# Optimization experiments

Hardware: AMD Instinct MI355X
Metric: run time of the kernel (lower is better)

Reference implementation:

```python
import jax, jax.numpy as jnp
import numpy as np

# Config (mirrors MarketBDHConfig / BDHConfig defaults used here)
B, T = 2, 512
NUM_ASSETS, IN_FEAT = 93, 4
D = 256          # n_embd
NH = 4           # n_head
MULT = 64        # mlp_internal_dim_multiplier
NL = 6           # n_layer
NI = D * MULT // NH  # per-head internal dim N = 4096
IN_DIM = NUM_ASSETS * IN_FEAT  # 372
ROPE_THETA = 2.0 ** 16
EPS = 1e-5


def _ln(x):
    # LayerNorm over last dim, elementwise_affine=False
    m = jnp.mean(x, axis=-1, keepdims=True)
    v = jnp.mean(jnp.square(x - m), axis=-1, keepdims=True)
    return (x - m) * jax.lax.rsqrt(v + EPS)


def _rope(x, cos, sin):
    # x: [B,NH,T,NI]; cos/sin: [T, NI//2] (broadcast over B,NH)
    x1, x2 = x[..., 0::2], x[..., 1::2]
    out = jnp.stack([x1 * cos - x2 * sin, x1 * sin + x2 * cos], axis=-1)
    return out.reshape(x.shape)


def setup_inputs() -> dict:
    key = jax.random.key(0)
    ks = jax.random.split(key, 9)
    s = 0.02
    return {
        "x": jax.random.normal(ks[0], (B, T, NUM_ASSETS, IN_FEAT), jnp.float32),
        "in_W": jax.random.normal(ks[1], (IN_DIM, D), jnp.float32) * s,
        "in_b": jnp.zeros((D,), jnp.float32),
        "encoder": jax.random.normal(ks[2], (NH, D, NI), jnp.float32) * s,
        "encoder_v": jax.random.normal(ks[3], (NH, D, NI), jnp.float32) * s,
        "decoder": jax.random.normal(ks[4], (NH * NI, D), jnp.float32) * s,
        "head_W": jax.random.normal(ks[5], (D, IN_DIM), jnp.float32) * s,
        "head_b": jnp.zeros((IN_DIM,), jnp.float32),
    }


def reference(x, in_W, in_b, encoder, encoder_v, decoder, head_W, head_b):
    # input projection: [B,T,N,F] -> [B,T,IN_DIM] -> [B,T,D]
    x_flat = x.reshape(B, T, IN_DIM)
    h = _ln(x_flat @ in_W + in_b)  # [B,T,D]

    # RoPE phase tables over the internal (latent) dimension
    freqs = 1.0 / (ROPE_THETA ** (jnp.arange(0, NI, 2, dtype=jnp.float32) / NI))
    phases = jnp.arange(T, dtype=jnp.float32)[:, None] * freqs[None, :]  # [T, NI/2]
    cos, sin = jnp.cos(phases), jnp.sin(phases)

    dec = decoder.reshape(NH, NI, D)  # head-major flatten matches transpose(1,2).reshape

    for _ in range(NL):
        h_res = h
        # encode + relu-sparsify: [B,NH,T,NI]
        h_sparse = jax.nn.relu(jnp.einsum('btd,hdn->bhtn', h, encoder))
        # BDH attention: linear (no softmax), K is Q, is_causal=False -> dense scores
        qr = _rope(h_sparse, cos, sin)
        scores = jnp.einsum('bhtn,bhsn->bhts', qr, qr)  # [B,NH,T,T]
        yKV = jnp.einsum('bhts,bsd->bhtd', scores, h)    # V = h broadcast over heads
        yKV = _ln(yKV)
        y_sparse = jax.nn.relu(jnp.einsum('bhtd,hdn->bhtn', yKV, encoder_v))
        xy_sparse = h_sparse * y_sparse  # multiplicative gating (dropout p=0)
        yMLP = jnp.einsum('bhtn,hnd->btd', xy_sparse, dec)
        h = _ln(h_res + _ln(yMLP))

    pred = (h @ head_W + head_b).reshape(B, T, NUM_ASSETS, IN_FEAT)
    return pred
```

## Files before the change

### kernel.cpp

```cpp
#include <hip/hip_runtime.h>
#include <math.h>

#define B_ 2
#define T_ 512
#define D_ 256
#define NH_ 4
#define NI_ 4096
#define IN_DIM_ 372
#define NL_ 6
#define EPS_ 1e-5f

typedef unsigned short u16;
typedef __attribute__((ext_vector_type(4))) float f32x4;
typedef __attribute__((ext_vector_type(8))) short bf16x8;

__device__ __forceinline__ u16 f2b(float f) {
  union { float f; unsigned u; } v; v.f = f;
  unsigned r = v.u + 0x7fffu + ((v.u >> 16) & 1u);
  return (u16)(r >> 16);
}
__device__ __forceinline__ float b2f(u16 s) {
  union { unsigned u; float f; } v; v.u = ((unsigned)s) << 16;
  return v.f;
}

__device__ __forceinline__ void gload16(const u16* g, u16* l) {
  __builtin_amdgcn_global_load_lds(
      (const __attribute__((address_space(1))) unsigned int*)g,
      (__attribute__((address_space(3))) unsigned int*)l, 16, 0, 0);
}

__device__ __forceinline__ float blkSum256(float v, float* sb4) {
  #pragma unroll
  for (int o = 32; o > 0; o >>= 1) v += __shfl_down(v, o, 64);
  int w = threadIdx.x >> 6;
  __syncthreads();
  if ((threadIdx.x & 63) == 0) sb4[w] = v;
  __syncthreads();
  return sb4[0] + sb4[1] + sb4[2] + sb4[3];
}

__device__ __forceinline__ void gemm128(const u16* __restrict__ A,
                                        const u16* __restrict__ Bt,
                                        int lda, int k0, int k1,
                                        int row0, int col0,
                                        u16* Als, u16* Bls,
                                        f32x4 acc[4][4]) {
  const int tid = threadIdx.x;
  const int lane = tid & 63;
  const int wv = tid >> 6;
  const int wr = (wv >> 1) << 6;
  const int wc = (wv & 1) << 6;
  const int frow = lane & 15;
  const int kch = (lane >> 4) << 3;
  #pragma unroll
  for (int m = 0; m < 4; m++)
    #pragma unroll
    for (int n = 0; n < 4; n++) {
      f32x4 z = {0.f, 0.f, 0.f, 0.f};
      acc[m][n] = z;
    }
  for (int k = k0; k < k1; k += 32) {
    #pragma unroll
    for (int i = 0; i < 2; i++) {
      int s = tid + (i << 8);
      int r = s >> 2, c = (s & 3) << 3;
      gload16(A + (long)(row0 + r) * lda + k + c, Als + s * 8);
      gload16(Bt + (long)(col0 + r) * lda + k + c, Bls + s * 8);
    }
    __syncthreads();
    bf16x8 af[4], bfv[4];
    #pragma unroll
    for (int m = 0; m < 4; m++)
      af[m] = *(const bf16x8*)(Als + (wr + m * 16 + frow) * 32 + kch);
    #pragma unroll
    for (int n = 0; n < 4; n++)
      bfv[n] = *(const bf16x8*)(Bls + (wc + n * 16 + frow) * 32 + kch);
    #pragma unroll
    for (int m = 0; m < 4; m++)
      #pragma unroll
      for (int n = 0; n < 4; n++)
        acc[m][n] = __builtin_amdgcn_mfma_f32_16x16x32_bf16(af[m], bfv[n], acc[m][n], 0, 0, 0);
    __syncthreads();
  }
}

#define EPILOG_SETUP \
  const int lane = threadIdx.x & 63; \
  const int wv = threadIdx.x >> 6; \
  const int wr = (wv >> 1) << 6, wc = (wv & 1) << 6;

#define STAGE_HALF(EXPR) \
  if (wr == h * 64) { \
    _Pragma("unroll") \
    for (int m = 0; m < 4; m++) \
      _Pragma("unroll") \
      for (int n = 0; n < 4; n++) \
        _Pragma("unroll") \
        for (int r = 0; r < 4; r++) { \
          int lr = m * 16 + ((lane >> 4) << 2) + r; \
          int lc = wc + n * 16 + (lane & 15); \
          float _a = acc[m][n][r]; \
          smem[lr * 128 + (lc ^ (((lr >> 2) & 7) << 3))] = f2b(EXPR); \
        } \
  } \
  __syncthreads();

__device__ __forceinline__ void storeC_lds(const f32x4 acc[4][4], u16* smem,
                                           u16* Cb, int ldc, int row0, int col0,
                                           int wr, int wc, int lane) {
  const int tid = threadIdx.x;
  #pragma unroll
  for (int h = 0; h < 2; h++) {
    STAGE_HALF(_a)
    #pragma unroll
    for (int i = 0; i < 4; i++) {
      int idx = i * 256 + tid;
      int lr = idx >> 4, ch = idx & 15;
      uint4 v = *(const uint4*)(smem + lr * 128 + ((ch ^ ((lr >> 2) & 7)) << 3));
      *(uint4*)(Cb + (long)(row0 + h * 64 + lr) * ldc + col0 + ch * 8) = v;
    }
    __syncthreads();
  }
}

__global__ __launch_bounds__(256)
void k_cs(unsigned* __restrict__ cs) {
  int idx = blockIdx.x * 256 + threadIdx.x;
  if (idx >= T_ * (NI_ / 2)) return;
  int t = idx >> 11;
  int k = idx & 2047;
  float freq = exp2f(-(float)k * (1.0f / 128.0f));
  float ph = (float)t * freq;
  cs[idx] = (unsigned)f2b(cosf(ph)) | ((unsigned)f2b(sinf(ph)) << 16);
}

__global__ __launch_bounds__(256)
void ktr(const float* __restrict__ src, u16* __restrict__ dst, int R, int C) {
  __shared__ float tile[64][65];
  long zoff = (long)blockIdx.z * R * C;
  int r0 = blockIdx.y * 64, c0 = blockIdx.x * 64;
  int tid = threadIdx.x;
  int tr = tid >> 4, tc4 = (tid & 15) * 4;
  #pragma unroll
  for (int i = 0; i < 4; i++) {
    int r = tr + i * 16;
    f32x4 v = *(const f32x4*)(src + zoff + (long)(r0 + r) * C + c0 + tc4);
    tile[r][tc4 + 0] = v.x; tile[r][tc4 + 1] = v.y;
    tile[r][tc4 + 2] = v.z; tile[r][tc4 + 3] = v.w;
  }
  __syncthreads();
  #pragma unroll
  for (int i = 0; i < 4; i++) {
    int c = tr + i * 16;
    ushort4 o;
    o.x = f2b(tile[tc4 + 0][c]); o.y = f2b(tile[tc4 + 1][c]);
    o.z = f2b(tile[tc4 + 2][c]); o.w = f2b(tile[tc4 + 3][c]);
    *(ushort4*)(dst + zoff + (long)(c0 + c) * R + r0 + tc4) = o;
  }
}

__global__ __launch_bounds__(256)
void k_input(const float* __restrict__ x, const float* __restrict__ W,
             const float* __restrict__ b, float* __restrict__ hf,
             u16* __restrict__ hbf, u16* __restrict__ hT) {
  __shared__ float xr[IN_DIM_];
  __shared__ float sb[4];
  int bt = blockIdx.x;
  int d = threadIdx.x;
  const float* xrow = x + (long)bt * IN_DIM_;
  for (int k = d; k < IN_DIM_; k += 256) xr[k] = xrow[k];
  __syncthreads();
  float acc = b[d];
  for (int k = 0; k < IN_DIM_; k++) acc += xr[k] * W[k * D_ + d];
  float mean = blkSum256(acc, sb) * (1.0f / D_);
  float c = acc - mean;
  float var = blkSum256(c * c, sb) * (1.0f / D_);
  float out = c * rsqrtf(var + EPS_);
  hf[(long)bt * D_ + d] = out;
  hbf[(long)bt * D_ + d] = f2b(out);
  hT[((long)(bt >> 9) * D_ + d) * T_ + (bt & 511)] = f2b(out);
}

__global__ __launch_bounds__(256)
void g_enc(const u16* __restrict__ hbf, const u16* __restrict__ enct,
           const unsigned* __restrict__ cs, u16* __restrict__ qr) {
  __shared__ u16 smem[8192];
  int head = blockIdx.z;
  int row0 = blockIdx.y * 128, col0 = blockIdx.x * 128;
  f32x4 acc[4][4];
  gemm128(hbf, enct + (long)head * NI_ * D_, D_, 0, D_, row0, col0,
          smem, smem + 4096, acc);
  EPILOG_SETUP
  const int tid = threadIdx.x;
  #pragma unroll
  for (int h = 0; h < 2; h++) {
    STAGE_HALF(fmaxf(_a, 0.f))
    #pragma unroll
    for (int i = 0; i < 4; i++) {
      int idx = i * 256 + tid;
      int lr = idx >> 4, ch = idx & 15;
      uint4 v = *(const uint4*)(smem + lr * 128 + ((ch ^ ((lr >> 2) & 7)) << 3));
      int gr = row0 + h * 64 + lr;
      int b = gr >> 9, t = gr & 511;
      int gcol = col0 + ch * 8;
      uint4 csv = *(const uint4*)(cs + (long)t * (NI_ / 2) + (gcol >> 1));
      const unsigned* pv = &v.x; const unsigned* pc = &csv.x;
      unsigned o[4];
      #pragma unroll
      for (int j = 0; j < 4; j++) {
        float v0 = b2f((u16)pv[j]), v1 = b2f((u16)(pv[j] >> 16));
        float cc = b2f((u16)pc[j]), ss = b2f((u16)(pc[j] >> 16));
        o[j] = (unsigned)f2b(v0 * cc - v1 * ss) | ((unsigned)f2b(v0 * ss + v1 * cc) << 16);
      }
      long qri = (((long)(b * NH_ + head)) * T_ + t) * NI_ + gcol;
      *(uint4*)(qr + qri) = make_uint4(o[0], o[1], o[2], o[3]);
    }
    __syncthreads();
  }
}

__global__ __launch_bounds__(256)
void g_scores(const u16* __restrict__ qr, u16* __restrict__ scpb) {
  __shared__ u16 smem[8192];
  int z2 = blockIdx.z;
  int z = z2 >> 2, ks = z2 & 3;
  const u16* A = qr + (long)z * T_ * NI_;
  int row0 = blockIdx.y * 128, col0 = blockIdx.x * 128;
  f32x4 acc[4][4];
  gemm128(A, A, NI_, ks * 1024, ks * 1024 + 1024, row0, col0,
          smem, smem + 4096, acc);
  EPILOG_SETUP
  storeC_lds(acc, smem, scpb + (long)(ks * 8 + z) * T_ * T_, T_, row0, col0, wr, wc, lane);
}

__global__ __launch_bounds__(256)
void k_scred(const u16* __restrict__ scpb, u16* __restrict__ scb) {
  const long SL = (long)8 * T_ * T_;
  long base = ((long)blockIdx.x * 256 + threadIdx.x) * 8;
  uint4 p0 = *(const uint4*)(scpb + base);
  uint4 p1 = *(const uint4*)(scpb + SL + base);
  uint4 p2 = *(const uint4*)(scpb + 2 * SL + base);
  uint4 p3 = *(const uint4*)(scpb + 3 * SL + base);
  unsigned o[4];
  const unsigned* a = &p0.x; const unsigned* bq = &p1.x;
  const unsigned* c = &p2.x; const unsigned* d = &p3.x;
  #pragma unroll
  for (int i = 0; i < 4; i++) {
    float lo = b2f((u16)a[i]) + b2f((u16)bq[i]) + b2f((u16)c[i]) + b2f((u16)d[i]);
    float hi = b2f((u16)(a[i] >> 16)) + b2f((u16)(bq[i] >> 16)) +
               b2f((u16)(c[i] >> 16)) + b2f((u16)(d[i] >> 16));
    o[i] = (unsigned)f2b(lo) | ((unsigned)f2b(hi) << 16);
  }
  *(uint4*)(scb + base) = make_uint4(o[0], o[1], o[2], o[3]);
}

__global__ __launch_bounds__(256)
void g_ykv(const u16* __restrict__ scb, const u16* __restrict__ hT,
           u16* __restrict__ ykvpb) {
  __shared__ u16 smem[8192];
  int z2 = blockIdx.z;
  int z = z2 >> 2, ks = z2 & 3;
  int b = z >> 2;
  int row0 = blockIdx.y * 128, col0 = blockIdx.x * 128;
  f32x4 acc[4][4];
  gemm128(scb + (long)z * T_ * T_, hT + (long)b * D_ * T_, T_,
          ks * 128, ks * 128 + 128, row0, col0, smem, smem + 4096, acc);
  EPILOG_SETUP
  storeC_lds(acc, smem, ykvpb + (long)(ks * 8 + z) * T_ * D_, D_, row0, col0, wr, wc, lane);
}

__global__ __launch_bounds__(256)
void k_lnykv(const u16* __restrict__ ykvpb, u16* __restrict__ ykvb) {
  __shared__ float sb[4];
  int blk = blockIdx.x;
  int d = threadIdx.x;
  const long SL = (long)8 * T_ * D_;
  long base = (long)blk * D_ + d;
  float acc = b2f(ykvpb[base]) + b2f(ykvpb[SL + base]) +
              b2f(ykvpb[2 * SL + base]) + b2f(ykvpb[3 * SL + base]);
  float mean = blkSum256(acc, sb) * (1.0f / D_);
  float c = acc - mean;
  float var = blkSum256(c * c, sb) * (1.0f / D_);
  ykvb[base] = f2b(c * rsqrtf(var + EPS_));
}

__global__ __launch_bounds__(256)
void g_ysp(const u16* __restrict__ ykvb, const u16* __restrict__ encvt,
           const u16* __restrict__ qr, const unsigned* __restrict__ cs,
           u16* __restrict__ xy) {
  __shared__ u16 smem[8192];
  int z = blockIdx.z;
  int b = z >> 2, head = z & 3;
  int row0 = blockIdx.y * 128, col0 = blockIdx.x * 128;
  f32x4 acc[4][4];
  gemm128(ykvb + (long)z * T_ * D_, encvt + (long)head * NI_ * D_, D_,
          0, D_, row0, col0, smem, smem + 4096, acc);
  EPILOG_SETUP
  const int tid = threadIdx.x;
  #pragma unroll
  for (int h = 0; h < 2; h++) {
    STAGE_HALF(fmaxf(_a, 0.f))
    #pragma unroll
    for (int i = 0; i < 4; i++) {
      int idx = i * 256 + tid;
      int lr = idx >> 4, ch = idx & 15;
      uint4 v = *(const uint4*)(smem + lr * 128 + ((ch ^ ((lr >> 2) & 7)) << 3));
      int t = row0 + h * 64 + lr;
      int gcol = col0 + ch * 8;
      uint4 qv = *(const uint4*)(qr + ((long)z * T_ + t) * NI_ + gcol);
      uint4 csv = *(const uint4*)(cs + (long)t * (NI_ / 2) + (gcol >> 1));
      const unsigned* pv = &v.x; const unsigned* pq = &qv.x; const unsigned* pc = &csv.x;
      unsigned o[4];
      #pragma unroll
      for (int j = 0; j < 4; j++) {
        float v0 = b2f((u16)pv[j]), v1 = b2f((u16)(pv[j] >> 16));
        float q0 = b2f((u16)pq[j]), q1 = b2f((u16)(pq[j] >> 16));
        float cc = b2f((u16)pc[j]), ss = b2f((u16)(pc[j] >> 16));
        float hs0 = fmaxf(cc * q0 + ss * q1, 0.f);
        float hs1 = fmaxf(cc * q1 - ss * q0, 0.f);
        o[j] = (unsigned)f2b(hs0 * v0) | ((unsigned)f2b(hs1 * v1) << 16);
      }
      long xyi = ((long)b * T_ + t) * (NH_ * NI_) + head * NI_ + gcol;
      *(uint4*)(xy + xyi) = make_uint4(o[0], o[1], o[2], o[3]);
    }
    __syncthreads();
  }
}

__global__ __launch_bounds__(256)
void g_ymlp(const u16* __restrict__ xy, const u16* __restrict__ dect,
            u16* __restrict__ ymlppb) {
  __shared__ u16 smem[8192];
  int ks = blockIdx.z;
  int row0 = blockIdx.y * 128, col0 = blockIdx.x * 128;
  f32x4 acc[4][4];
  gemm128(xy, dect, NH_ * NI_, ks * 1024, ks * 1024 + 1024, row0, col0,
          smem, smem + 4096, acc);
  EPILOG_SETUP
  storeC_lds(acc, smem, ymlppb + (long)ks * (B_ * T_) * D_, D_, row0, col0, wr, wc, lane);
}

__global__ __launch_bounds__(256)
void k_dln(const u16* __restrict__ ymlppb, float* __restrict__ hf,
           u16* __restrict__ hbf, u16* __restrict__ hT) {
  __shared__ float sb[4];
  int bt = blockIdx.x;
  int d = threadIdx.x;
  const long SL = (long)(B_ * T_) * D_;
  float acc = 0.f;
  #pragma unroll
  for (int p = 0; p < 16; p++)
    acc += b2f(ymlppb[p * SL + (long)bt * D_ + d]);
  float mean = blkSum256(acc, sb) * (1.0f / D_);
  float c = acc - mean;
  float var = blkSum256(c * c, sb) * (1.0f / D_);
  float u = c * rsqrtf(var + EPS_);
  float v2 = hf[(long)bt * D_ + d] + u;
  float m2 = blkSum256(v2, sb) * (1.0f / D_);
  float c2 = v2 - m2;
  float va2 = blkSum256(c2 * c2, sb) * (1.0f / D_);
  float out = c2 * rsqrtf(va2 + EPS_);
  hf[(long)bt * D_ + d] = out;
  hbf[(long)bt * D_ + d] = f2b(out);
  hT[((long)(bt >> 9) * D_ + d) * T_ + (bt & 511)] = f2b(out);
}

__global__ __launch_bounds__(384)
void k_head(const float* __restrict__ h, const float* __restrict__ W,
            const float* __restrict__ bb, float* __restrict__ out) {
  __shared__ float hr[D_];
  int bt = blockIdx.x;
  int j = threadIdx.x;
  for (int k = j; k < D_; k += 384) hr[k] = h[(long)bt * D_ + k];
  __syncthreads();
  if (j < IN_DIM_) {
    float acc = bb[j];
    for (int d2 = 0; d2 < D_; d2++) acc += hr[d2] * W[(long)d2 * IN_DIM_ + j];
    out[(long)bt * IN_DIM_ + j] = acc;
  }
}

extern "C" void kernel_launch(void* const* d_in, const int* in_sizes, int n_in,
                              void* d_out, int out_size, void* d_ws, size_t ws_size,
                              hipStream_t stream) {
  const float* x    = (const float*)d_in[0];
  const float* in_W = (const float*)d_in[1];
  const float* in_b = (const float*)d_in[2];
  const float* enc  = (const float*)d_in[3];
  const float* encv = (const float*)d_in[4];
  const float* dec  = (const float*)d_in[5];
  const float* hW   = (const float*)d_in[6];
  const float* hb   = (const float*)d_in[7];
  float* out = (float*)d_out;

  char* p = (char*)d_ws;
  auto alloc = [&](size_t bytes) { char* r = p; p += (bytes + 255) & ~(size_t)255; return r; };
  unsigned* cs   = (unsigned*)alloc((size_t)T_ * (NI_ / 2) * 4);
  float* hf      = (float*)alloc((size_t)B_ * T_ * D_ * 4);
  u16*   hbf     = (u16*)  alloc((size_t)B_ * T_ * D_ * 2);
  u16*   hT      = (u16*)  alloc((size_t)B_ * D_ * T_ * 2);
  u16*   enct    = (u16*)  alloc((size_t)NH_ * D_ * NI_ * 2);
  u16*   encvt   = (u16*)  alloc((size_t)NH_ * D_ * NI_ * 2);
  u16*   dect    = (u16*)  alloc((size_t)NH_ * NI_ * D_ * 2);
  u16*   qr      = (u16*)  alloc((size_t)B_ * NH_ * T_ * NI_ * 2);
  u16*   xy      = (u16*)  alloc((size_t)B_ * T_ * NH_ * NI_ * 2);
  u16*   scpb    = (u16*)  alloc((size_t)4 * 8 * T_ * T_ * 2);
  u16*   scb     = (u16*)  alloc((size_t)8 * T_ * T_ * 2);
  u16*   ykvpb   = (u16*)  alloc((size_t)4 * 8 * T_ * D_ * 2);
  u16*   ykvb    = (u16*)  alloc((size_t)8 * T_ * D_ * 2);
  u16*   ymlppb  = (u16*)  alloc((size_t)16 * B_ * T_ * D_ * 2);

  k_cs<<<dim3(4096), dim3(256), 0, stream>>>(cs);
  ktr<<<dim3(NI_ / 64, D_ / 64, NH_), dim3(256), 0, stream>>>(enc, enct, D_, NI_);
  ktr<<<dim3(NI_ / 64, D_ / 64, NH_), dim3(256), 0, stream>>>(encv, encvt, D_, NI_);
  ktr<<<dim3(D_ / 64, (NH_ * NI_) / 64, 1), dim3(256), 0, stream>>>(dec, dect, NH_ * NI_, D_);
  k_input<<<dim3(B_ * T_), dim3(256), 0, stream>>>(x, in_W, in_b, hf, hbf, hT);

  for (int l = 0; l < NL_; l++) {
    g_enc<<<dim3(32, 8, 4), dim3(256), 0, stream>>>(hbf, enct, cs, qr);
    g_scores<<<dim3(4, 4, 32), dim3(256), 0, stream>>>(qr, scpb);
    k_scred<<<dim3(1024), dim3(256), 0, stream>>>(scpb, scb);
    g_ykv<<<dim3(2, 4, 32), dim3(256), 0, stream>>>(scb, hT, ykvpb);
    k_lnykv<<<dim3(B_ * NH_ * T_), dim3(256), 0, stream>>>(ykvpb, ykvb);
    g_ysp<<<dim3(32, 4, 8), dim3(256), 0, stream>>>(ykvb, encvt, qr, cs, xy);
    g_ymlp<<<dim3(2, 8, 16), dim3(256), 0, stream>>>(xy, dect, ymlppb);
    k_dln<<<dim3(B_ * T_), dim3(256), 0, stream>>>(ymlppb, hf, hbf, hT);
  }

  k_head<<<dim3(B_ * T_), dim3(384), 0, stream>>>(hf, hW, hb, out);
}
```

Before: 816.2 us.

## Double GEMM K-step to 64 with XOR-swizzled LDS and fuse split-K score reduction

The shared GEMM tile loop now stages 64-wide K slices instead of 32, with an XOR swizzle on the LDS column chunks to avoid bank conflicts. It issues two MFMA rounds per barrier pair, halving syncs per K. The split-K score partial reduction is folded into the ykv GEMM's A-tile load, which removes the k_scred kernel and the intermediate scores buffer round trip. LDS use per block doubles, which may reduce occupancy, and ykv blocks now each re-read four partial score slices.

```diff
diff --git a/kernel.cpp b/kernel.cpp
--- a/kernel.cpp
+++ b/kernel.cpp
@@ -52,7 +52,8 @@
   const int wr = (wv >> 1) << 6;
   const int wc = (wv & 1) << 6;
   const int frow = lane & 15;
-  const int kch = (lane >> 4) << 3;
+  const int kg = lane >> 4;
+  const int sw = frow & 7;
   #pragma unroll
   for (int m = 0; m < 4; m++)
     #pragma unroll
@@ -60,27 +61,32 @@
       f32x4 z = {0.f, 0.f, 0.f, 0.f};
       acc[m][n] = z;
     }
-  for (int k = k0; k < k1; k += 32) {
-    #pragma unroll
-    for (int i = 0; i < 2; i++) {
+  for (int k = k0; k < k1; k += 64) {
+    #pragma unroll
+    for (int i = 0; i < 4; i++) {
       int s = tid + (i << 8);
-      int r = s >> 2, c = (s & 3) << 3;
+      int r = s >> 3;
+      int c = (((s & 7) ^ (r & 7)) << 3);
       gload16(A + (long)(row0 + r) * lda + k + c, Als + s * 8);
       gload16(Bt + (long)(col0 + r) * lda + k + c, Bls + s * 8);
     }
     __syncthreads();
-    bf16x8 af[4], bfv[4];
-    #pragma unroll
-    for (int m = 0; m < 4; m++)
-      af[m] = *(const bf16x8*)(Als + (wr + m * 16 + frow) * 32 + kch);
-    #pragma unroll
-    for (int n = 0; n < 4; n++)
-      bfv[n] = *(const bf16x8*)(Bls + (wc + n * 16 + frow) * 32 + kch);
-    #pragma unroll
-    for (int m = 0; m < 4; m++)
+    #pragma unroll
+    for (int kk = 0; kk < 2; kk++) {
+      const int slot = ((((kk << 2) + kg) ^ sw) << 3);
+      bf16x8 af[4], bfv[4];
+      #pragma unroll
+      for (int m = 0; m < 4; m++)
+        af[m] = *(const bf16x8*)(Als + (wr + m * 16 + frow) * 64 + slot);
       #pragma unroll
       for (int n = 0; n < 4; n++)
-        acc[m][n] = __builtin_amdgcn_mfma_f32_16x16x32_bf16(af[m], bfv[n], acc[m][n], 0, 0, 0);
+        bfv[n] = *(const bf16x8*)(Bls + (wc + n * 16 + frow) * 64 + slot);
+      #pragma unroll
+      for (int m = 0; m < 4; m++)
+        #pragma unroll
+        for (int n = 0; n < 4; n++)
+          acc[m][n] = __builtin_amdgcn_mfma_f32_16x16x32_bf16(af[m], bfv[n], acc[m][n], 0, 0, 0);
+    }
     __syncthreads();
   }
 }
@@ -185,12 +191,12 @@
 __global__ __launch_bounds__(256)
 void g_enc(const u16* __restrict__ hbf, const u16* __restrict__ enct,
            const unsigned* __restrict__ cs, u16* __restrict__ qr) {
-  __shared__ u16 smem[8192];
+  __shared__ u16 smem[16384];
   int head = blockIdx.z;
   int row0 = blockIdx.y * 128, col0 = blockIdx.x * 128;
   f32x4 acc[4][4];
   gemm128(hbf, enct + (long)head * NI_ * D_, D_, 0, D_, row0, col0,
-          smem, smem + 4096, acc);
+          smem, smem + 8192, acc);
   EPILOG_SETUP
   const int tid = threadIdx.x;
   #pragma unroll
@@ -222,51 +228,96 @@
 
 __global__ __launch_bounds__(256)
 void g_scores(const u16* __restrict__ qr, u16* __restrict__ scpb) {
-  __shared__ u16 smem[8192];
+  __shared__ u16 smem[16384];
   int z2 = blockIdx.z;
   int z = z2 >> 2, ks = z2 & 3;
   const u16* A = qr + (long)z * T_ * NI_;
   int row0 = blockIdx.y * 128, col0 = blockIdx.x * 128;
   f32x4 acc[4][4];
   gemm128(A, A, NI_, ks * 1024, ks * 1024 + 1024, row0, col0,
-          smem, smem + 4096, acc);
+          smem, smem + 8192, acc);
   EPILOG_SETUP
   storeC_lds(acc, smem, scpb + (long)(ks * 8 + z) * T_ * T_, T_, row0, col0, wr, wc, lane);
 }
 
 __global__ __launch_bounds__(256)
-void k_scred(const u16* __restrict__ scpb, u16* __restrict__ scb) {
-  const long SL = (long)8 * T_ * T_;
-  long base = ((long)blockIdx.x * 256 + threadIdx.x) * 8;
-  uint4 p0 = *(const uint4*)(scpb + base);
-  uint4 p1 = *(const uint4*)(scpb + SL + base);
-  uint4 p2 = *(const uint4*)(scpb + 2 * SL + base);
-  uint4 p3 = *(const uint4*)(scpb + 3 * SL + base);
-  unsigned o[4];
-  const unsigned* a = &p0.x; const unsigned* bq = &p1.x;
-  const unsigned* c = &p2.x; const unsigned* d = &p3.x;
-  #pragma unroll
-  for (int i = 0; i < 4; i++) {
-    float lo = b2f((u16)a[i]) + b2f((u16)bq[i]) + b2f((u16)c[i]) + b2f((u16)d[i]);
-    float hi = b2f((u16)(a[i] >> 16)) + b2f((u16)(bq[i] >> 16)) +
-               b2f((u16)(c[i] >> 16)) + b2f((u16)(d[i] >> 16));
-    o[i] = (unsigned)f2b(lo) | ((unsigned)f2b(hi) << 16);
-  }
-  *(uint4*)(scb + base) = make_uint4(o[0], o[1], o[2], o[3]);
-}
-
-__global__ __launch_bounds__(256)
-void g_ykv(const u16* __restrict__ scb, const u16* __restrict__ hT,
+void g_ykv(const u16* __restrict__ scpb, const u16* __restrict__ hT,
            u16* __restrict__ ykvpb) {
-  __shared__ u16 smem[8192];
+  __shared__ u16 smem[16384];
+  u16* Als = smem;
+  u16* Bls = smem + 8192;
   int z2 = blockIdx.z;
   int z = z2 >> 2, ks = z2 & 3;
   int b = z >> 2;
   int row0 = blockIdx.y * 128, col0 = blockIdx.x * 128;
+  const long SL = (long)8 * T_ * T_;
+  const u16* Ab = scpb + (long)z * T_ * T_;
+  const u16* Bt = hT + (long)b * D_ * T_;
+  const int tid = threadIdx.x;
+  const int lane = tid & 63;
+  const int wv = tid >> 6;
+  const int wr = (wv >> 1) << 6, wc = (wv & 1) << 6;
+  const int frow = lane & 15;
+  const int kg = lane >> 4;
+  const int sw = frow & 7;
   f32x4 acc[4][4];
-  gemm128(scb + (long)z * T_ * T_, hT + (long)b * D_ * T_, T_,
-          ks * 128, ks * 128 + 128, row0, col0, smem, smem + 4096, acc);
-  EPILOG_SETUP
+  #pragma unroll
+  for (int m = 0; m < 4; m++)
+    #pragma unroll
+    for (int n = 0; n < 4; n++) {
+      f32x4 zz = {0.f, 0.f, 0.f, 0.f};
+      acc[m][n] = zz;
+    }
+  const int ar = tid >> 1;
+  const int ac0 = (tid & 1) << 2;
+  for (int k = ks * 128; k < ks * 128 + 128; k += 64) {
+    long gb = (long)(row0 + ar) * T_ + k;
+    #pragma unroll
+    for (int j = 0; j < 4; j++) {
+      int jj = ac0 + j;
+      long ga = gb + (jj << 3);
+      uint4 p0 = *(const uint4*)(Ab + ga);
+      uint4 p1 = *(const uint4*)(Ab + SL + ga);
+      uint4 p2 = *(const uint4*)(Ab + 2 * SL + ga);
+      uint4 p3 = *(const uint4*)(Ab + 3 * SL + ga);
+      const unsigned* q0 = &p0.x; const unsigned* q1 = &p1.x;
+      const unsigned* q2 = &p2.x; const unsigned* q3 = &p3.x;
+      unsigned o[4];
+      #pragma unroll
+      for (int w = 0; w < 4; w++) {
+        float lo = b2f((u16)q0[w]) + b2f((u16)q1[w]) + b2f((u16)q2[w]) + b2f((u16)q3[w]);
+        float hi = b2f((u16)(q0[w] >> 16)) + b2f((u16)(q1[w] >> 16)) +
+                   b2f((u16)(q2[w] >> 16)) + b2f((u16)(q3[w] >> 16));
+        o[w] = (unsigned)f2b(lo) | ((unsigned)f2b(hi) << 16);
+      }
+      *(uint4*)(Als + ar * 64 + ((jj ^ (ar & 7)) << 3)) = make_uint4(o[0], o[1], o[2], o[3]);
+    }
+    #pragma unroll
+    for (int i = 0; i < 4; i++) {
+      int s = tid + (i << 8);
+      int r = s >> 3;
+      int c = (((s & 7) ^ (r & 7)) << 3);
+      gload16(Bt + (long)(col0 + r) * T_ + k + c, Bls + s * 8);
+    }
+    __syncthreads();
+    #pragma unroll
+    for (int kk = 0; kk < 2; kk++) {
+      const int slot = ((((kk << 2) + kg) ^ sw) << 3);
+      bf16x8 af[4], bfv[4];
+      #pragma unroll
+      for (int m = 0; m < 4; m++)
+        af[m] = *(const bf16x8*)(Als + (wr + m * 16 + frow) * 64 + slot);
+      #pragma unroll
+      for (int n = 0; n < 4; n++)
+        bfv[n] = *(const bf16x8*)(Bls + (wc + n * 16 + frow) * 64 + slot);
+      #pragma unroll
+      for (int m = 0; m < 4; m++)
+        #pragma unroll
+        for (int n = 0; n < 4; n++)
+          acc[m][n] = __builtin_amdgcn_mfma_f32_16x16x32_bf16(af[m], bfv[n], acc[m][n], 0, 0, 0);
+    }
+    __syncthreads();
+  }
   storeC_lds(acc, smem, ykvpb + (long)(ks * 8 + z) * T_ * D_, D_, row0, col0, wr, wc, lane);
 }
 
@@ -289,13 +340,13 @@
 void g_ysp(const u16* __restrict__ ykvb, const u16* __restrict__ encvt,
            const u16* __restrict__ qr, const unsigned* __restrict__ cs,
            u16* __restrict__ xy) {
-  __shared__ u16 smem[8192];
+  __shared__ u16 smem[16384];
   int z = blockIdx.z;
   int b = z >> 2, head = z & 3;
   int row0 = blockIdx.y * 128, col0 = blockIdx.x * 128;
   f32x4 acc[4][4];
   gemm128(ykvb + (long)z * T_ * D_, encvt + (long)head * NI_ * D_, D_,
-          0, D_, row0, col0, smem, smem + 4096, acc);
+          0, D_, row0, col0, smem, smem + 8192, acc);
   EPILOG_SETUP
   const int tid = threadIdx.x;
   #pragma unroll
@@ -331,12 +382,12 @@
 __global__ __launch_bounds__(256)
 void g_ymlp(const u16* __restrict__ xy, const u16* __restrict__ dect,
             u16* __restrict__ ymlppb) {
-  __shared__ u16 smem[8192];
+  __shared__ u16 smem[16384];
   int ks = blockIdx.z;
   int row0 = blockIdx.y * 128, col0 = blockIdx.x * 128;
   f32x4 acc[4][4];
   gemm128(xy, dect, NH_ * NI_, ks * 1024, ks * 1024 + 1024, row0, col0,
-          smem, smem + 4096, acc);
+          smem, smem + 8192, acc);
   EPILOG_SETUP
   storeC_lds(acc, smem, ymlppb + (long)ks * (B_ * T_) * D_, D_, row0, col0, wr, wc, lane);
 }
@@ -406,7 +457,6 @@
   u16*   qr      = (u16*)  alloc((size_t)B_ * NH_ * T_ * NI_ * 2);
   u16*   xy      = (u16*)  alloc((size_t)B_ * T_ * NH_ * NI_ * 2);
   u16*   scpb    = (u16*)  alloc((size_t)4 * 8 * T_ * T_ * 2);
-  u16*   scb     = (u16*)  alloc((size_t)8 * T_ * T_ * 2);
   u16*   ykvpb   = (u16*)  alloc((size_t)4 * 8 * T_ * D_ * 2);
   u16*   ykvb    = (u16*)  alloc((size_t)8 * T_ * D_ * 2);
   u16*   ymlppb  = (u16*)  alloc((size_t)16 * B_ * T_ * D_ * 2);
@@ -420,8 +470,7 @@
   for (int l = 0; l < NL_; l++) {
     g_enc<<<dim3(32, 8, 4), dim3(256), 0, stream>>>(hbf, enct, cs, qr);
     g_scores<<<dim3(4, 4, 32), dim3(256), 0, stream>>>(qr, scpb);
-    k_scred<<<dim3(1024), dim3(256), 0, stream>>>(scpb, scb);
-    g_ykv<<<dim3(2, 4, 32), dim3(256), 0, stream>>>(scb, hT, ykvpb);
+    g_ykv<<<dim3(2, 4, 32), dim3(256), 0, stream>>>(scpb, hT, ykvpb);
     k_lnykv<<<dim3(B_ * NH_ * T_), dim3(256), 0, stream>>>(ykvpb, ykvb);
     g_ysp<<<dim3(32, 4, 8), dim3(256), 0, stream>>>(ykvb, encvt, qr, cs, xy);
     g_ymlp<<<dim3(2, 8, 16), dim3(256), 0, stream>>>(xy, dect, ymlppb);
```

Measured after the change: 798.4 us. 2.2% less time.
